# Kernel tuning notes

Measured on AMD Instinct MI355X. Metric: run time of the kernel, lower is better.

Reference implementation:

```python
import jax, jax.numpy as jnp
import numpy as np

N_NODES = 100000
N_EDGES = 2000000
H = 128


def setup_inputs() -> dict:
    key = jax.random.key(0)
    ks = jax.random.split(key, 5)
    z_src = jax.random.normal(ks[0], (N_NODES, H), dtype=jnp.float32)
    z_dst = jax.random.normal(ks[1], (N_NODES, H), dtype=jnp.float32)
    edge_label_index = jax.random.randint(ks[2], (2, N_EDGES), 0, N_NODES, dtype=jnp.int64)
    # Linear(2H, H) and Linear(H, 1) params (stored as [in, out] for x @ W)
    W1 = jax.random.normal(ks[3], (2 * H, H), dtype=jnp.float32) * (1.0 / np.sqrt(2 * H))
    b1 = jnp.zeros((H,), dtype=jnp.float32)
    W2 = jax.random.normal(ks[4], (H, 1), dtype=jnp.float32) * (1.0 / np.sqrt(H))
    b2 = jnp.zeros((1,), dtype=jnp.float32)
    return {"z_src": z_src, "z_dst": z_dst, "edge_label_index": edge_label_index,
            "W1": W1, "b1": b1, "W2": W2, "b2": b2}


def reference(z_src, z_dst, edge_label_index, W1, b1, W2, b2):
    row, col = edge_label_index[0], edge_label_index[1]
    # gather + concat -> [E, 2H]
    z = jnp.concatenate([z_src[row], z_dst[col]], axis=-1)
    h = jax.nn.relu(z @ W1 + b1)          # [E, H]
    out = h @ W2 + b2                     # [E, 1]
    return out.reshape(-1)
```

## Files before the change

### kernel.cpp

```cpp
#include <hip/hip_runtime.h>

#define HDIM 128

typedef __bf16 bf16_t;
typedef bf16_t bf16x8 __attribute__((ext_vector_type(8)));
typedef float  f32x4  __attribute__((ext_vector_type(4)));

__device__ __forceinline__ unsigned short f2bf_rne(float f) {
    unsigned int u = __float_as_uint(f);
    u += 0x7fffu + ((u >> 16) & 1u);
    return (unsigned short)(u >> 16);
}
__device__ __forceinline__ unsigned int pk_bf2(float a, float b) {
    return (unsigned int)f2bf_rne(a) | ((unsigned int)f2bf_rne(b) << 16);
}

__global__ __launch_bounds__(256) void convert_w1(
    const float* __restrict__ W1, unsigned short* __restrict__ Wt)
{
    const int o = blockIdx.x * 256 + threadIdx.x;
    const int g = o >> 14, rem = o & 16383, n = rem >> 7, k = rem & 127;
    Wt[o] = f2bf_rne(W1[g * 16384 + k * 128 + n]);
}

__global__ __launch_bounds__(256) void node_gemm_v6(
    const float* __restrict__ Zs, const float* __restrict__ Zd,
    const unsigned short* __restrict__ Wt, const float* __restrict__ b1,
    unsigned short* __restrict__ Abuf, unsigned short* __restrict__ Bbuf,
    int M, int tiles_per_half)
{
    __shared__ unsigned short wlds[128 * 128];

    const bool second = (blockIdx.x >= tiles_per_half);
    const int tile = second ? (blockIdx.x - tiles_per_half) : blockIdx.x;
    const float* __restrict__ Z          = second ? Zd : Zs;
    const unsigned short* __restrict__ W = Wt + (second ? 128 * 128 : 0);
    unsigned short* __restrict__ C       = second ? Bbuf : Abuf;
    const int t    = threadIdx.x;
    const int lane = t & 63;
    const int wave = t >> 6;
    const int m    = lane & 15;
    const int quad = lane >> 4;

    const int r  = tile * 64 + wave * 16 + m;
    const int rc = (r < M) ? r : (M - 1);
    const float* zrow = Z + (size_t)rc * HDIM;
    float4 zv[4][2];
    #pragma unroll
    for (int ks = 0; ks < 4; ++ks) {
        zv[ks][0] = *reinterpret_cast<const float4*>(zrow + ks * 32 + quad * 8);
        zv[ks][1] = *reinterpret_cast<const float4*>(zrow + ks * 32 + quad * 8 + 4);
    }

    #pragma unroll
    for (int j = 0; j < 8; ++j) {
        const int u = t + 256 * j;
        const int n = u >> 4, cc = u & 15;
        const uint4 v = *reinterpret_cast<const uint4*>(W + n * 128 + cc * 8);
        *reinterpret_cast<uint4*>(wlds + n * 128 + (cc ^ (n & 7)) * 8) = v;
    }
    __syncthreads();

    union { unsigned int u[4]; bf16x8 h; } zf[4];
    #pragma unroll
    for (int ks = 0; ks < 4; ++ks) {
        zf[ks].u[0] = pk_bf2(zv[ks][0].x, zv[ks][0].y);
        zf[ks].u[1] = pk_bf2(zv[ks][0].z, zv[ks][0].w);
        zf[ks].u[2] = pk_bf2(zv[ks][1].x, zv[ks][1].y);
        zf[ks].u[3] = pk_bf2(zv[ks][1].z, zv[ks][1].w);
    }

    f32x4 acc[8] = {};
    #pragma unroll
    for (int ks = 0; ks < 4; ++ks) {
        const int cidx = (ks * 4 + quad) ^ (m & 7);
        #pragma unroll
        for (int ct = 0; ct < 8; ++ct) {
            const bf16x8 wf = *reinterpret_cast<const bf16x8*>(
                wlds + (ct * 16 + m) * 128 + cidx * 8);
            acc[ct] = __builtin_amdgcn_mfma_f32_16x16x32_bf16(
                wf, zf[ks].h, acc[ct], 0, 0, 0);
        }
    }

    if (r < M) {
        unsigned short* crow = C + (size_t)r * HDIM;
        #pragma unroll
        for (int ct = 0; ct < 8; ++ct) {
            const int col = ct * 16 + quad * 4;
            float4 bv = make_float4(0.f, 0.f, 0.f, 0.f);
            if (second) bv = *reinterpret_cast<const float4*>(b1 + col);
            uint2 o;
            o.x = pk_bf2(acc[ct][0] + bv.x, acc[ct][1] + bv.y);
            o.y = pk_bf2(acc[ct][2] + bv.z, acc[ct][3] + bv.w);
            *reinterpret_cast<uint2*>(crow + col) = o;
        }
    }
}

__global__ __launch_bounds__(256) void edge_decode_bf16(
    const unsigned short* __restrict__ A, const unsigned short* __restrict__ Bm,
    const int* __restrict__ idx,
    const float* __restrict__ W2, const float* __restrict__ b2,
    float* __restrict__ out, int E)
{
    const int t   = threadIdx.x;
    const int sub = t & 15;
    const int grp = t >> 4;

    float w2r[8];
    #pragma unroll
    for (int i = 0; i < 8; ++i) w2r[i] = W2[sub * 8 + i];
    const float b2s = b2[0];

    const int stride = gridDim.x * 16;
    for (int e = blockIdx.x * 16 + grp; e < E; e += stride) {
        const int r = idx[e];
        const int c = idx[E + e];
        const uint4 av = *reinterpret_cast<const uint4*>(A  + (size_t)r * HDIM + sub * 8);
        const uint4 bv = *reinterpret_cast<const uint4*>(Bm + (size_t)c * HDIM + sub * 8);

        float s = 0.f;
        #pragma unroll
        for (int i = 0; i < 4; ++i) {
            const unsigned int ua = (&av.x)[i];
            const unsigned int ub = (&bv.x)[i];
            s += fmaxf(__uint_as_float(ua << 16)         + __uint_as_float(ub << 16),         0.f) * w2r[2 * i];
            s += fmaxf(__uint_as_float(ua & 0xffff0000u) + __uint_as_float(ub & 0xffff0000u), 0.f) * w2r[2 * i + 1];
        }
        s += __shfl_xor(s, 1);
        s += __shfl_xor(s, 2);
        s += __shfl_xor(s, 4);
        s += __shfl_xor(s, 8);
        if (sub == 0) out[e] = s + b2s;
    }
}

extern "C" void kernel_launch(void* const* d_in, const int* in_sizes, int n_in,
                              void* d_out, int out_size, void* d_ws, size_t ws_size,
                              hipStream_t stream)
{
    const float* z_src = (const float*)d_in[0];
    const float* z_dst = (const float*)d_in[1];
    const int*   eidx  = (const int*)d_in[2];
    const float* W1    = (const float*)d_in[3];
    const float* b1    = (const float*)d_in[4];
    const float* W2    = (const float*)d_in[5];
    const float* b2    = (const float*)d_in[6];
    float*       outp  = (float*)d_out;

    const int Nn = in_sizes[0] / HDIM;
    const int E  = in_sizes[2] / 2;

    unsigned short* Abuf = (unsigned short*)d_ws;
    unsigned short* Bbuf = Abuf + (size_t)Nn * HDIM;
    unsigned short* Wt   = Bbuf + (size_t)Nn * HDIM;

    convert_w1<<<128, 256, 0, stream>>>(W1, Wt);

    const int tiles = (Nn + 63) >> 6;
    node_gemm_v6<<<2 * tiles, 256, 0, stream>>>(
        z_src, z_dst, Wt, b1, Abuf, Bbuf, Nn, tiles);

    edge_decode_bf16<<<8192, 256, 0, stream>>>(Abuf, Bbuf, eidx, W2, b2, outp, E);
}
```

Measured before the change: 291.4 us.

## Process four row tiles per block in node GEMM with double-buffered Z loads

The node GEMM block now handles 256 rows in four 64-row steps instead of one 64-row tile. The 32 KB weight staging into LDS is amortised over four tiles, and the next tile's Z rows are prefetched into registers while the current tile runs its MFMAs. This cuts the grid size by four and raises register pressure from the doubled zv buffers, which could lower occupancy.

New measurement: 299.9 us. +2.9%, slower.

```diff
diff --git a/kernel.cpp b/kernel.cpp
--- a/kernel.cpp
+++ b/kernel.cpp
@@ -23,16 +23,16 @@
     Wt[o] = f2bf_rne(W1[g * 16384 + k * 128 + n]);
 }
 
-__global__ __launch_bounds__(256) void node_gemm_v6(
+__global__ __launch_bounds__(256) void node_gemm_v7(
     const float* __restrict__ Zs, const float* __restrict__ Zd,
     const unsigned short* __restrict__ Wt, const float* __restrict__ b1,
     unsigned short* __restrict__ Abuf, unsigned short* __restrict__ Bbuf,
-    int M, int tiles_per_half)
+    int M, int blocks_per_half)
 {
     __shared__ unsigned short wlds[128 * 128];
 
-    const bool second = (blockIdx.x >= tiles_per_half);
-    const int tile = second ? (blockIdx.x - tiles_per_half) : blockIdx.x;
+    const bool second = (blockIdx.x >= blocks_per_half);
+    const int blk = second ? (blockIdx.x - blocks_per_half) : blockIdx.x;
     const float* __restrict__ Z          = second ? Zd : Zs;
     const unsigned short* __restrict__ W = Wt + (second ? 128 * 128 : 0);
     unsigned short* __restrict__ C       = second ? Bbuf : Abuf;
@@ -41,16 +41,6 @@
     const int wave = t >> 6;
     const int m    = lane & 15;
     const int quad = lane >> 4;
-
-    const int r  = tile * 64 + wave * 16 + m;
-    const int rc = (r < M) ? r : (M - 1);
-    const float* zrow = Z + (size_t)rc * HDIM;
-    float4 zv[4][2];
-    #pragma unroll
-    for (int ks = 0; ks < 4; ++ks) {
-        zv[ks][0] = *reinterpret_cast<const float4*>(zrow + ks * 32 + quad * 8);
-        zv[ks][1] = *reinterpret_cast<const float4*>(zrow + ks * 32 + quad * 8 + 4);
-    }
 
     #pragma unroll
     for (int j = 0; j < 8; ++j) {
@@ -61,39 +51,71 @@
     }
     __syncthreads();
 
-    union { unsigned int u[4]; bf16x8 h; } zf[4];
-    #pragma unroll
-    for (int ks = 0; ks < 4; ++ks) {
-        zf[ks].u[0] = pk_bf2(zv[ks][0].x, zv[ks][0].y);
-        zf[ks].u[1] = pk_bf2(zv[ks][0].z, zv[ks][0].w);
-        zf[ks].u[2] = pk_bf2(zv[ks][1].x, zv[ks][1].y);
-        zf[ks].u[3] = pk_bf2(zv[ks][1].z, zv[ks][1].w);
-    }
+    const int row_base = blk * 256 + wave * 16 + m;
 
-    f32x4 acc[8] = {};
-    #pragma unroll
-    for (int ks = 0; ks < 4; ++ks) {
-        const int cidx = (ks * 4 + quad) ^ (m & 7);
+    float4 zv[2][4][2];
+
+    {
+        const int r  = row_base;
+        const int rc = (r < M) ? r : (M - 1);
+        const float* zrow = Z + (size_t)rc * HDIM;
         #pragma unroll
-        for (int ct = 0; ct < 8; ++ct) {
-            const bf16x8 wf = *reinterpret_cast<const bf16x8*>(
-                wlds + (ct * 16 + m) * 128 + cidx * 8);
-            acc[ct] = __builtin_amdgcn_mfma_f32_16x16x32_bf16(
-                wf, zf[ks].h, acc[ct], 0, 0, 0);
+        for (int ks = 0; ks < 4; ++ks) {
+            zv[0][ks][0] = *reinterpret_cast<const float4*>(zrow + ks * 32 + quad * 8);
+            zv[0][ks][1] = *reinterpret_cast<const float4*>(zrow + ks * 32 + quad * 8 + 4);
         }
     }
 
-    if (r < M) {
-        unsigned short* crow = C + (size_t)r * HDIM;
+    #pragma unroll
+    for (int st = 0; st < 4; ++st) {
+        const int cur = st & 1;
+
+        if (st < 3) {
+            const int rn  = row_base + (st + 1) * 64;
+            const int rnc = (rn < M) ? rn : (M - 1);
+            const float* zrow = Z + (size_t)rnc * HDIM;
+            #pragma unroll
+            for (int ks = 0; ks < 4; ++ks) {
+                zv[cur ^ 1][ks][0] = *reinterpret_cast<const float4*>(zrow + ks * 32 + quad * 8);
+                zv[cur ^ 1][ks][1] = *reinterpret_cast<const float4*>(zrow + ks * 32 + quad * 8 + 4);
+            }
+        }
+
+        union { unsigned int u[4]; bf16x8 h; } zf[4];
         #pragma unroll
-        for (int ct = 0; ct < 8; ++ct) {
-            const int col = ct * 16 + quad * 4;
-            float4 bv = make_float4(0.f, 0.f, 0.f, 0.f);
-            if (second) bv = *reinterpret_cast<const float4*>(b1 + col);
-            uint2 o;
-            o.x = pk_bf2(acc[ct][0] + bv.x, acc[ct][1] + bv.y);
-            o.y = pk_bf2(acc[ct][2] + bv.z, acc[ct][3] + bv.w);
-            *reinterpret_cast<uint2*>(crow + col) = o;
+        for (int ks = 0; ks < 4; ++ks) {
+            zf[ks].u[0] = pk_bf2(zv[cur][ks][0].x, zv[cur][ks][0].y);
+            zf[ks].u[1] = pk_bf2(zv[cur][ks][0].z, zv[cur][ks][0].w);
+            zf[ks].u[2] = pk_bf2(zv[cur][ks][1].x, zv[cur][ks][1].y);
+            zf[ks].u[3] = pk_bf2(zv[cur][ks][1].z, zv[cur][ks][1].w);
+        }
+
+        f32x4 acc[8] = {};
+        #pragma unroll
+        for (int ks = 0; ks < 4; ++ks) {
+            const int cidx = (ks * 4 + quad) ^ (m & 7);
+            #pragma unroll
+            for (int ct = 0; ct < 8; ++ct) {
+                const bf16x8 wf = *reinterpret_cast<const bf16x8*>(
+                    wlds + (ct * 16 + m) * 128 + cidx * 8);
+                acc[ct] = __builtin_amdgcn_mfma_f32_16x16x32_bf16(
+                    wf, zf[ks].h, acc[ct], 0, 0, 0);
+            }
+        }
+
+        const int r = row_base + st * 64;
+        if (r < M) {
+            unsigned short* crow = C + (size_t)r * HDIM;
+            #pragma unroll
+            for (int ct = 0; ct < 8; ++ct) {
+                const int col = ct * 16 + quad * 4;
+                float4 bv = make_float4(0.f, 0.f, 0.f, 0.f);
+                if (second) bv = *reinterpret_cast<const float4*>(b1 + col);
+                uint2 o;
+                o.x = pk_bf2(acc[ct][0] + bv.x, acc[ct][1] + bv.y);
+                o.y = pk_bf2(acc[ct][2] + bv.z, acc[ct][3] + bv.w);
+                *reinterpret_cast<uint2*>(crow + col) = o;
+            }
         }
     }
 }
@@ -158,9 +180,9 @@
 
     convert_w1<<<128, 256, 0, stream>>>(W1, Wt);
 
-    const int tiles = (Nn + 63) >> 6;
-    node_gemm_v6<<<2 * tiles, 256, 0, stream>>>(
-        z_src, z_dst, Wt, b1, Abuf, Bbuf, Nn, tiles);
+    const int bph = (Nn + 255) >> 8;
+    node_gemm_v7<<<2 * bph, 256, 0, stream>>>(
+        z_src, z_dst, Wt, b1, Abuf, Bbuf, Nn, bph);
 
     edge_decode_bf16<<<8192, 256, 0, stream>>>(Abuf, Bbuf, eidx, W2, b2, outp, E);
 }
```

## Fuse node GEMM and edge decode into one cooperative persistent kernel

Applied to the files above, without the earlier changes.

Replaces the separate node GEMM and edge decode launches with a single cooperative kernel of 1024 persistent blocks. Each block first loops over node tiles with W1 staged once in LDS, then all blocks meet at a grid-wide sync and run the gather-decode loop. This removes one kernel launch and lets the W1 LDS load be amortised across tiles. The cost is the grid barrier, less parallelism in the decode phase (1024 blocks instead of 8192), and a launch-bounds occupancy constraint. It falls back to the old two-kernel path if the cooperative launch fails.

Result: slower. 665.0 us (+128.2%).

```diff
diff --git a/kernel.cpp b/kernel.cpp
--- a/kernel.cpp
+++ b/kernel.cpp
@@ -1,6 +1,11 @@
 #include <hip/hip_runtime.h>
-
-#define HDIM 128
+#include <hip/hip_cooperative_groups.h>
+
+namespace cg = cooperative_groups;
+
+#define HDIM  128
+#define FBLKS 1024
+#define HBLKS (FBLKS / 2)
 
 typedef __bf16 bf16_t;
 typedef bf16_t bf16x8 __attribute__((ext_vector_type(8)));
@@ -21,6 +26,137 @@
     const int o = blockIdx.x * 256 + threadIdx.x;
     const int g = o >> 14, rem = o & 16383, n = rem >> 7, k = rem & 127;
     Wt[o] = f2bf_rne(W1[g * 16384 + k * 128 + n]);
+}
+
+__global__ __launch_bounds__(256, 4) void fused_gemm_decode(
+    const float* __restrict__ Zs, const float* __restrict__ Zd,
+    const unsigned short* __restrict__ Wt, const float* __restrict__ b1,
+    unsigned short* __restrict__ Abuf, unsigned short* __restrict__ Bbuf,
+    const int* __restrict__ idx, const float* __restrict__ W2,
+    const float* __restrict__ b2, float* __restrict__ out,
+    int M, int E, int tiles_per_half)
+{
+    __shared__ unsigned short wlds[128 * 128];
+
+    const int t    = threadIdx.x;
+    const int lane = t & 63;
+    const int wave = t >> 6;
+    const int m    = lane & 15;
+    const int quad = lane >> 4;
+
+    {
+        const bool second = (blockIdx.x >= HBLKS);
+        const int bx = second ? (blockIdx.x - HBLKS) : blockIdx.x;
+        const float* __restrict__ Z          = second ? Zd : Zs;
+        const unsigned short* __restrict__ W = Wt + (second ? 128 * 128 : 0);
+        unsigned short* __restrict__ C       = second ? Bbuf : Abuf;
+
+        float4 zv[4][2];
+        const bool has0 = (bx < tiles_per_half);
+        if (has0) {
+            const int r  = bx * 64 + wave * 16 + m;
+            const int rc = (r < M) ? r : (M - 1);
+            const float* zrow = Z + (size_t)rc * HDIM;
+            #pragma unroll
+            for (int ks = 0; ks < 4; ++ks) {
+                zv[ks][0] = *reinterpret_cast<const float4*>(zrow + ks * 32 + quad * 8);
+                zv[ks][1] = *reinterpret_cast<const float4*>(zrow + ks * 32 + quad * 8 + 4);
+            }
+        }
+
+        #pragma unroll
+        for (int j = 0; j < 8; ++j) {
+            const int u = t + 256 * j;
+            const int n = u >> 4, cc = u & 15;
+            const uint4 v = *reinterpret_cast<const uint4*>(W + n * 128 + cc * 8);
+            *reinterpret_cast<uint4*>(wlds + n * 128 + (cc ^ (n & 7)) * 8) = v;
+        }
+        __syncthreads();
+
+        for (int tile = bx; tile < tiles_per_half; tile += HBLKS) {
+            const int r  = tile * 64 + wave * 16 + m;
+            if (tile != bx) {
+                const int rc = (r < M) ? r : (M - 1);
+                const float* zrow = Z + (size_t)rc * HDIM;
+                #pragma unroll
+                for (int ks = 0; ks < 4; ++ks) {
+                    zv[ks][0] = *reinterpret_cast<const float4*>(zrow + ks * 32 + quad * 8);
+                    zv[ks][1] = *reinterpret_cast<const float4*>(zrow + ks * 32 + quad * 8 + 4);
+                }
+            }
+
+            union { unsigned int u[4]; bf16x8 h; } zf[4];
+            #pragma unroll
+            for (int ks = 0; ks < 4; ++ks) {
+                zf[ks].u[0] = pk_bf2(zv[ks][0].x, zv[ks][0].y);
+                zf[ks].u[1] = pk_bf2(zv[ks][0].z, zv[ks][0].w);
+                zf[ks].u[2] = pk_bf2(zv[ks][1].x, zv[ks][1].y);
+                zf[ks].u[3] = pk_bf2(zv[ks][1].z, zv[ks][1].w);
+            }
+
+            f32x4 acc[8] = {};
+            #pragma unroll
+            for (int ks = 0; ks < 4; ++ks) {
+                const int cidx = (ks * 4 + quad) ^ (m & 7);
+                #pragma unroll
+                for (int ct = 0; ct < 8; ++ct) {
+                    const bf16x8 wf = *reinterpret_cast<const bf16x8*>(
+                        wlds + (ct * 16 + m) * 128 + cidx * 8);
+                    acc[ct] = __builtin_amdgcn_mfma_f32_16x16x32_bf16(
+                        wf, zf[ks].h, acc[ct], 0, 0, 0);
+                }
+            }
+
+            if (r < M) {
+                unsigned short* crow = C + (size_t)r * HDIM;
+                #pragma unroll
+                for (int ct = 0; ct < 8; ++ct) {
+                    const int col = ct * 16 + quad * 4;
+                    float4 bv = make_float4(0.f, 0.f, 0.f, 0.f);
+                    if (second) bv = *reinterpret_cast<const float4*>(b1 + col);
+                    uint2 o;
+                    o.x = pk_bf2(acc[ct][0] + bv.x, acc[ct][1] + bv.y);
+                    o.y = pk_bf2(acc[ct][2] + bv.z, acc[ct][3] + bv.w);
+                    *reinterpret_cast<uint2*>(crow + col) = o;
+                }
+            }
+        }
+    }
+
+    __threadfence();
+    cg::this_grid().sync();
+
+    {
+        const int sub = t & 15;
+        const int grp = t >> 4;
+
+        float w2r[8];
+        #pragma unroll
+        for (int i = 0; i < 8; ++i) w2r[i] = W2[sub * 8 + i];
+        const float b2s = b2[0];
+
+        const int stride = FBLKS * 16;
+        for (int e = blockIdx.x * 16 + grp; e < E; e += stride) {
+            const int r = idx[e];
+            const int c = idx[E + e];
+            const uint4 av = *reinterpret_cast<const uint4*>(Abuf + (size_t)r * HDIM + sub * 8);
+            const uint4 bv = *reinterpret_cast<const uint4*>(Bbuf + (size_t)c * HDIM + sub * 8);
+
+            float s = 0.f;
+            #pragma unroll
+            for (int i = 0; i < 4; ++i) {
+                const unsigned int ua = (&av.x)[i];
+                const unsigned int ub = (&bv.x)[i];
+                s += fmaxf(__uint_as_float(ua << 16)         + __uint_as_float(ub << 16),         0.f) * w2r[2 * i];
+                s += fmaxf(__uint_as_float(ua & 0xffff0000u) + __uint_as_float(ub & 0xffff0000u), 0.f) * w2r[2 * i + 1];
+            }
+            s += __shfl_xor(s, 1);
+            s += __shfl_xor(s, 2);
+            s += __shfl_xor(s, 4);
+            s += __shfl_xor(s, 8);
+            if (sub == 0) out[e] = s + b2s;
+        }
+    }
 }
 
 __global__ __launch_bounds__(256) void node_gemm_v6(
@@ -159,8 +295,22 @@
     convert_w1<<<128, 256, 0, stream>>>(W1, Wt);
 
     const int tiles = (Nn + 63) >> 6;
-    node_gemm_v6<<<2 * tiles, 256, 0, stream>>>(
-        z_src, z_dst, Wt, b1, Abuf, Bbuf, Nn, tiles);
-
-    edge_decode_bf16<<<8192, 256, 0, stream>>>(Abuf, Bbuf, eidx, W2, b2, outp, E);
-}
+
+    const float* Zs_ = z_src;  const float* Zd_ = z_dst;
+    const unsigned short* Wt_ = Wt;  const float* b1_ = b1;
+    unsigned short* A_ = Abuf; unsigned short* B_ = Bbuf;
+    const int* idx_ = eidx;    const float* W2_ = W2; const float* b2_ = b2;
+    float* out_ = outp;        int M_ = Nn; int E_ = E; int tl_ = tiles;
+    void* args[] = { &Zs_, &Zd_, &Wt_, &b1_, &A_, &B_, &idx_, &W2_, &b2_,
+                     &out_, &M_, &E_, &tl_ };
+    hipError_t err = hipLaunchCooperativeKernel(
+        reinterpret_cast<const void*>(fused_gemm_decode),
+        dim3(FBLKS), dim3(256), args, 0, stream);
+
+    if (err != hipSuccess) {
+        node_gemm_v6<<<2 * tiles, 256, 0, stream>>>(
+            z_src, z_dst, Wt, b1, Abuf, Bbuf, Nn, tiles);
+        edge_decode_bf16<<<8192, 256, 0, stream>>>(
+            Abuf, Bbuf, eidx, W2, b2, outp, E);
+    }
+}
```

## Bucket edges by source row before decoding to improve gather locality

Applied to the files above, without the earlier changes.

Adds a counting-sort pipeline (histogram, scan, scatter) that groups edges into buckets of 128 source rows. Each decode group then walks a contiguous chunk of edges, so the A-row gathers hit cache more often, and results are written back through the original edge index. The cost is four extra kernel launches, atomics on bucket offsets, extra workspace and extra index traffic, plus scattered output writes. The old path is kept as a fallback when the workspace is too small.

Measured after the change: 789.5 us. 2.71x slower.

```diff
diff --git a/kernel.cpp b/kernel.cpp
--- a/kernel.cpp
+++ b/kernel.cpp
@@ -1,6 +1,8 @@
 #include <hip/hip_runtime.h>
 
 #define HDIM 128
+#define NB   1024
+#define BSH  7
 
 typedef __bf16 bf16_t;
 typedef bf16_t bf16x8 __attribute__((ext_vector_type(8)));
@@ -98,6 +100,99 @@
     }
 }
 
+__global__ __launch_bounds__(256) void zero_cnt(int* __restrict__ p, int n)
+{
+    const int i = blockIdx.x * 256 + threadIdx.x;
+    if (i < n) p[i] = 0;
+}
+
+__global__ __launch_bounds__(256) void edge_hist(
+    const int* __restrict__ rows, int* __restrict__ cnt, int E)
+{
+    __shared__ int h[NB];
+    for (int i = threadIdx.x; i < NB; i += 256) h[i] = 0;
+    __syncthreads();
+    for (int e = blockIdx.x * 256 + threadIdx.x; e < E; e += gridDim.x * 256)
+        atomicAdd(&h[rows[e] >> BSH], 1);
+    __syncthreads();
+    for (int i = threadIdx.x; i < NB; i += 256) {
+        const int v = h[i];
+        if (v) atomicAdd(&cnt[i], v);
+    }
+}
+
+__global__ __launch_bounds__(NB) void scan_off(
+    const int* __restrict__ cnt, int* __restrict__ off)
+{
+    __shared__ int s[NB];
+    const int t = threadIdx.x;
+    const int c0 = cnt[t];
+    s[t] = c0;
+    __syncthreads();
+    for (int d = 1; d < NB; d <<= 1) {
+        const int v = (t >= d) ? s[t - d] : 0;
+        __syncthreads();
+        s[t] += v;
+        __syncthreads();
+    }
+    off[t] = s[t] - c0;
+}
+
+__global__ __launch_bounds__(256) void edge_scatter(
+    const int* __restrict__ rows, const int* __restrict__ cols,
+    int* __restrict__ off, int2* __restrict__ rc, int* __restrict__ og, int E)
+{
+    for (int e = blockIdx.x * 256 + threadIdx.x; e < E; e += gridDim.x * 256) {
+        const int r = rows[e];
+        const int c = cols[e];
+        const int p = atomicAdd(&off[r >> BSH], 1);
+        if (p < E) {
+            rc[p] = make_int2(r, c);
+            og[p] = e;
+        }
+    }
+}
+
+__global__ __launch_bounds__(256) void edge_decode_sorted(
+    const unsigned short* __restrict__ A, const unsigned short* __restrict__ Bm,
+    const int2* __restrict__ rc, const int* __restrict__ og,
+    const float* __restrict__ W2, const float* __restrict__ b2,
+    float* __restrict__ out, int E, int chunk)
+{
+    const int t   = threadIdx.x;
+    const int sub = t & 15;
+    const int grp = t >> 4;
+
+    float w2r[8];
+    #pragma unroll
+    for (int i = 0; i < 8; ++i) w2r[i] = W2[sub * 8 + i];
+    const float b2s = b2[0];
+
+    const int gid = blockIdx.x * 16 + grp;
+    const int i0  = gid * chunk;
+    const int i1  = min(i0 + chunk, E);
+
+    for (int i = i0; i < i1; ++i) {
+        const int2 p = rc[i];
+        const uint4 av = *reinterpret_cast<const uint4*>(A  + (size_t)p.x * HDIM + sub * 8);
+        const uint4 bv = *reinterpret_cast<const uint4*>(Bm + (size_t)p.y * HDIM + sub * 8);
+
+        float s = 0.f;
+        #pragma unroll
+        for (int k = 0; k < 4; ++k) {
+            const unsigned int ua = (&av.x)[k];
+            const unsigned int ub = (&bv.x)[k];
+            s += fmaxf(__uint_as_float(ua << 16)         + __uint_as_float(ub << 16),         0.f) * w2r[2 * k];
+            s += fmaxf(__uint_as_float(ua & 0xffff0000u) + __uint_as_float(ub & 0xffff0000u), 0.f) * w2r[2 * k + 1];
+        }
+        s += __shfl_xor(s, 1);
+        s += __shfl_xor(s, 2);
+        s += __shfl_xor(s, 4);
+        s += __shfl_xor(s, 8);
+        if (sub == 0) out[og[i]] = s + b2s;
+    }
+}
+
 __global__ __launch_bounds__(256) void edge_decode_bf16(
     const unsigned short* __restrict__ A, const unsigned short* __restrict__ Bm,
     const int* __restrict__ idx,
@@ -155,6 +250,12 @@
     unsigned short* Abuf = (unsigned short*)d_ws;
     unsigned short* Bbuf = Abuf + (size_t)Nn * HDIM;
     unsigned short* Wt   = Bbuf + (size_t)Nn * HDIM;
+    int*  cnt = (int*)(Wt + 2 * 128 * 128);
+    int*  off = cnt + NB;
+    int2* rc  = (int2*)(off + NB);
+    int*  og  = (int*)(rc + (size_t)E);
+
+    const size_t need = (size_t)((char*)(og + E) - (char*)d_ws);
 
     convert_w1<<<128, 256, 0, stream>>>(W1, Wt);
 
@@ -162,5 +263,17 @@
     node_gemm_v6<<<2 * tiles, 256, 0, stream>>>(
         z_src, z_dst, Wt, b1, Abuf, Bbuf, Nn, tiles);
 
-    edge_decode_bf16<<<8192, 256, 0, stream>>>(Abuf, Bbuf, eidx, W2, b2, outp, E);
-}
+    if (ws_size >= need) {
+        zero_cnt<<<(2 * NB + 255) / 256, 256, 0, stream>>>(cnt, 2 * NB);
+        edge_hist<<<512, 256, 0, stream>>>(eidx, cnt, E);
+        scan_off<<<1, NB, 0, stream>>>(cnt, off);
+        edge_scatter<<<2048, 256, 0, stream>>>(eidx, eidx + E, off, rc, og, E);
+        const int groups = 8192 * 16;
+        const int chunk  = (E + groups - 1) / groups;
+        edge_decode_sorted<<<8192, 256, 0, stream>>>(
+            Abuf, Bbuf, rc, og, W2, b2, outp, E, chunk);
+    } else {
+        edge_decode_bf16<<<8192, 256, 0, stream>>>(
+            Abuf, Bbuf, eidx, W2, b2, outp, E);
+    }
+}
```
